# Kernel optimization log

Measured on AMD Instinct MI355X. Metric: run time of the kernel, lower is better.

The kernel has to match this reference:

```python
import jax, jax.numpy as jnp
import numpy as np

N_TAG = 128
START = 126  # tag2idx[START_TAG]
STOP = 127   # tag2idx[STOP_TAG]
NEG_INF = -10000.0


def setup_inputs() -> dict:
    key = jax.random.key(0)
    k1, k2, k3 = jax.random.split(key, 3)
    B, T = 512, 512
    feats = jax.random.normal(k1, (B, T, N_TAG), dtype=jnp.float32)
    transitions = jax.random.normal(k2, (N_TAG, N_TAG), dtype=jnp.float32)
    # __init__ constraints: no transition into START, none out of STOP
    transitions = transitions.at[START, :].set(NEG_INF)
    transitions = transitions.at[:, STOP].set(NEG_INF)
    tags = jax.random.randint(k3, (B, T), 0, 126, dtype=jnp.int32)
    return {"feats": feats, "transitions": transitions, "tags": tags}


def reference(feats, transitions, tags):
    # feats: [B, T, N], transitions[i, j] = score(j -> i), tags: [B, T]
    B, T, N = feats.shape

    # ---- forward algorithm (batched log-sum-exp DP) ----
    init = jnp.full((B, N), NEG_INF, dtype=feats.dtype).at[:, START].set(0.0)

    def step(fv, feat_t):  # fv: [B, N] (alpha over prev tag j), feat_t: [B, N]
        # tag_var[b, i, j] = fv[b, j] + transitions[i, j] + feat_t[b, i]
        tag_var = fv[:, None, :] + transitions[None, :, :] + feat_t[:, :, None]
        return jax.nn.logsumexp(tag_var, axis=2), None

    fv, _ = jax.lax.scan(step, init, jnp.swapaxes(feats, 0, 1))  # scan over T
    forward_score = jax.nn.logsumexp(fv + transitions[STOP][None, :], axis=1)  # [B]

    # ---- gold path score ----
    start_col = jnp.full((B, 1), START, dtype=tags.dtype)
    stop_col = jnp.full((B, 1), STOP, dtype=tags.dtype)
    pad_start = jnp.concatenate([start_col, tags], axis=1)  # from-tags, [B, T+1]
    pad_stop = jnp.concatenate([tags, stop_col], axis=1)    # to-tags,   [B, T+1]
    trans_score = transitions[pad_stop, pad_start].sum(axis=1)  # [B]
    emit_score = jnp.take_along_axis(feats, tags[:, :, None].astype(jnp.int32), axis=2)[..., 0].sum(axis=1)
    gold_score = trans_score + emit_score

    # negative log-likelihood per sequence
    return forward_score - gold_score
```

## Files before the change

### kernel.cpp

```cpp
#include <hip/hip_runtime.h>
#include <hip/hip_bf16.h>

#define N_TAG 128
#define T_LEN 512
#define START_TAG 126
#define STOP_TAG 127

typedef __attribute__((ext_vector_type(8))) __bf16 bf16x8;
typedef __attribute__((ext_vector_type(4))) float f32x4;

__global__ __launch_bounds__(320, 1)
void crf_split_kernel(const float* __restrict__ feats,
                      const float* __restrict__ trans,
                      const int* __restrict__ tags,
                      float* __restrict__ out) {
  const int tid = threadIdx.x;
  const int wid = tid >> 6;
  const int lane = tid & 63;
  const int bbase = blockIdx.x * 2;

  __shared__ float Uf[2][N_TAG];
  __shared__ float Wb[2][N_TAG];
  __shared__ float LZ[4];
  __shared__ float GOLD[2];

  if (wid == 4) {
    const int half = lane >> 5, tl = lane & 31;
    const int b = bbase + half;
    const int* tg = tags + (size_t)b * T_LEN;
    const float* fg = feats + (size_t)b * T_LEN * N_TAG;
    float gsum = 0.f;
    for (int t = tl; t < T_LEN; t += 32) {
      int tag = tg[t];
      int prev = (t == 0) ? START_TAG : tg[t - 1];
      gsum += trans[(size_t)tag * N_TAG + prev] + fg[(size_t)t * N_TAG + tag];
      if (t == T_LEN - 1) gsum += trans[STOP_TAG * N_TAG + tag];
    }
#pragma unroll
    for (int s = 16; s; s >>= 1) gsum += __shfl_xor(gsum, s);
    if (tl == 0) GOLD[half] = gsum;
    __syncthreads();
#pragma unroll
    for (int bL = 0; bL < 2; ++bL) {
      float sd = Uf[bL][lane] * Wb[bL][lane] +
                 Uf[bL][lane + 64] * Wb[bL][lane + 64];
#pragma unroll
      for (int s = 32; s; s >>= 1) sd += __shfl_xor(sd, s);
      if (lane == 0)
        out[bbase + bL] = __logf(sd) + LZ[2 * bL] + LZ[2 * bL + 1] - GOLD[bL];
    }
    return;
  }

  const int bL = wid >> 1, dir = wid & 1;
  const int batch = bbase + bL;
  const int n = lane & 15, g = lane >> 4;
  const float* fbase = feats + (size_t)batch * T_LEN * N_TAG;
  const int T0 = dir ? 510 : 0;
  const int TS = dir ? -1 : 1;
  const int ib = 32 * g;

  bf16x8 A[8][4];
#pragma unroll
  for (int mt = 0; mt < 8; ++mt) {
    const int tau = 32 * (mt >> 1) + 8 * (n >> 2) + 4 * (mt & 1) + (n & 3);
#pragma unroll
    for (int kk = 0; kk < 4; ++kk) {
      bf16x8 v;
      if (dir == 0) {
        const float* p = trans + (size_t)tau * N_TAG + 32 * kk + 8 * g;
        f32x4 x = *(const f32x4*)p;
        f32x4 y = *(const f32x4*)(p + 4);
        v[0] = (__bf16)__expf(x[0]); v[1] = (__bf16)__expf(x[1]);
        v[2] = (__bf16)__expf(x[2]); v[3] = (__bf16)__expf(x[3]);
        v[4] = (__bf16)__expf(y[0]); v[5] = (__bf16)__expf(y[1]);
        v[6] = (__bf16)__expf(y[2]); v[7] = (__bf16)__expf(y[3]);
      } else {
#pragma unroll
        for (int j = 0; j < 8; ++j)
          v[j] = (__bf16)__expf(trans[(size_t)(32 * kk + 8 * g + j) * N_TAG + tau]);
      }
      A[mt][kk] = v;
    }
  }

  bf16x8 Bv[4];
#pragma unroll
  for (int kk = 0; kk < 4; ++kk) {
    bf16x8 z;
#pragma unroll
    for (int j = 0; j < 8; ++j) z[j] = (__bf16)0.0f;
    Bv[kk] = z;
  }
  if (dir == 0) {
    if (g == 3) Bv[3][6] = (__bf16)1.0f;
  } else {
    const float* s127 = trans + (size_t)STOP_TAG * N_TAG;
    const float* f511 = fbase + (size_t)(T_LEN - 1) * N_TAG;
#pragma unroll
    for (int kk = 0; kk < 4; ++kk) {
      const int off = 32 * kk + 8 * g;
      f32x4 s0 = *(const f32x4*)(s127 + off);
      f32x4 s1 = *(const f32x4*)(s127 + off + 4);
      f32x4 e0 = *(const f32x4*)(f511 + off);
      f32x4 e1 = *(const f32x4*)(f511 + off + 4);
      bf16x8 v;
      v[0] = (__bf16)__expf(s0[0] + e0[0]); v[1] = (__bf16)__expf(s0[1] + e0[1]);
      v[2] = (__bf16)__expf(s0[2] + e0[2]); v[3] = (__bf16)__expf(s0[3] + e0[3]);
      v[4] = (__bf16)__expf(s1[0] + e1[0]); v[5] = (__bf16)__expf(s1[1] + e1[1]);
      v[6] = (__bf16)__expf(s1[2] + e1[2]); v[7] = (__bf16)__expf(s1[3] + e1[3]);
      Bv[kk] = v;
    }
  }

  float Lr[4][2];
#pragma unroll
  for (int s = 0; s < 4; ++s) {
    const float* rp = fbase + (size_t)(T0 + TS * s) * N_TAG;
    Lr[s][0] = rp[lane];
    Lr[s][1] = rp[lane + 64];
  }
  Lr[0][0] = __expf(Lr[0][0]);
  Lr[0][1] = __expf(Lr[0][1]);
  float logZ = 0.0f;

#define BPERM(DST, SLOT)                                                     \
  {                                                                          \
    _Pragma("unroll") for (int a = 0; a < 4; ++a) {                          \
      int sv_ = __float_as_int((a < 2) ? Lr[SLOT][0] : Lr[SLOT][1]);         \
      _Pragma("unroll") for (int bb = 0; bb < 2; ++bb) {                     \
        _Pragma("unroll") for (int r = 0; r < 4; ++r) {                      \
          int w_ = __builtin_amdgcn_ds_bpermute(                             \
              ib + 128 * (a & 1) + 16 * bb + 4 * r, sv_);                    \
          DST[2 * a + bb][r] = __int_as_float(w_);                           \
        }                                                                    \
      }                                                                      \
    }                                                                        \
  }

#define RENORM(ACC)                                                          \
  {                                                                          \
    float mx_ = ACC[0][0];                                                   \
    _Pragma("unroll") for (int mt = 0; mt < 8; ++mt)                         \
        mx_ = fmaxf(mx_, fmaxf(fmaxf(ACC[mt][0], ACC[mt][1]),                \
                               fmaxf(ACC[mt][2], ACC[mt][3])));              \
    mx_ = fmaxf(mx_, __shfl_xor(mx_, 16));                                   \
    mx_ = fmaxf(mx_, __shfl_xor(mx_, 32));                                   \
    int eb_ = __float_as_int(mx_) & 0x7f800000;                              \
    float inv_ = __int_as_float(0x7f000000 - eb_);           \
    logZ += (float)((eb_ >> 23) - 127) * 0.69314718056f;                     \
    _Pragma("unroll") for (int mt = 0; mt < 8; ++mt) {                       \
      ACC[mt][0] *= inv_; ACC[mt][1] *= inv_;                                \
      ACC[mt][2] *= inv_; ACC[mt][3] *= inv_;                                \
    }                                                                        \
  }

#define ITER(S, SX, KP4, DOREN)                                              \
  {                                                                          \
    f32x4 EF[8];                                                             \
    BPERM(EF, S);                                                            \
    f32x4 acc[8];                                                            \
    _Pragma("unroll") for (int mt = 0; mt < 8; ++mt)                         \
        acc[mt] = (f32x4){0.f, 0.f, 0.f, 0.f};                               \
    _Pragma("unroll") for (int kk = 0; kk < 4; ++kk) {                       \
      _Pragma("unroll") for (int mt = 0; mt < 8; ++mt)                       \
          acc[mt] = __builtin_amdgcn_mfma_f32_16x16x32_bf16(                 \
              A[mt][kk], Bv[kk], acc[mt], 0, 0, 0);                          \
    }                                                                        \
    _Pragma("unroll") for (int mt = 0; mt < 8; ++mt) {                       \
      acc[mt][0] *= EF[mt][0]; acc[mt][1] *= EF[mt][1];                      \
      acc[mt][2] *= EF[mt][2]; acc[mt][3] *= EF[mt][3];                      \
    }                                                                        \
    if (DOREN) RENORM(acc);                                                  \
    _Pragma("unroll") for (int kk = 0; kk < 4; ++kk) {                       \
      bf16x8 nb;                                                             \
      nb[0] = (__bf16)acc[2 * kk][0];     nb[1] = (__bf16)acc[2 * kk][1];    \
      nb[2] = (__bf16)acc[2 * kk][2];     nb[3] = (__bf16)acc[2 * kk][3];    \
      nb[4] = (__bf16)acc[2 * kk + 1][0]; nb[5] = (__bf16)acc[2 * kk + 1][1];\
      nb[6] = (__bf16)acc[2 * kk + 1][2]; nb[7] = (__bf16)acc[2 * kk + 1][3];\
      Bv[kk] = nb;                                                           \
    }                                                                        \
    Lr[SX][0] = __expf(Lr[SX][0]);  \
    Lr[SX][1] = __expf(Lr[SX][1]);                                           \
    {                                                                        \
      const float* rp_ = fbase + (size_t)(T0 + TS * (KP4)) * N_TAG;          \
      Lr[S][0] = rp_[lane];               \
      Lr[S][1] = rp_[lane + 64];                                             \
    }                                                                        \
  }

  for (int kb = 0; kb < 63; ++kb) {
    const int k0 = kb * 4;
    ITER(0, 1, k0 + 4, false);
    ITER(1, 2, k0 + 5, false);
    ITER(2, 3, k0 + 6, false);
    ITER(3, 0, k0 + 7, true);
  }
  ITER(0, 1, 256, false);
  ITER(1, 2, 257, false);
  ITER(2, 3, 258, false);

  f32x4 upF[8];
  {
    f32x4 EF[8];
    BPERM(EF, 3);
    f32x4 acc[8];
#pragma unroll
    for (int mt = 0; mt < 8; ++mt) acc[mt] = (f32x4){0.f, 0.f, 0.f, 0.f};
#pragma unroll
    for (int kk = 0; kk < 4; ++kk) {
#pragma unroll
      for (int mt = 0; mt < 8; ++mt)
        acc[mt] = __builtin_amdgcn_mfma_f32_16x16x32_bf16(A[mt][kk], Bv[kk],
                                                          acc[mt], 0, 0, 0);
    }
    if (dir == 0) {
#pragma unroll
      for (int mt = 0; mt < 8; ++mt) {
        acc[mt][0] *= EF[mt][0]; acc[mt][1] *= EF[mt][1];
        acc[mt][2] *= EF[mt][2]; acc[mt][3] *= EF[mt][3];
      }
    }
    RENORM(acc);
#pragma unroll
    for (int mt = 0; mt < 8; ++mt) upF[mt] = acc[mt];
  }

  float* dst = (dir == 0) ? Uf[bL] : Wb[bL];
  if (n == 0) {
#pragma unroll
    for (int mt = 0; mt < 8; ++mt) {
      const int base = 32 * (mt >> 1) + 8 * g + 4 * (mt & 1);
#pragma unroll
      for (int r = 0; r < 4; ++r) dst[base + r] = upF[mt][r];
    }
  }
  if (lane == 0) LZ[wid] = logZ;
  __syncthreads();
#undef ITER
#undef RENORM
#undef BPERM
}

extern "C" void kernel_launch(void* const* d_in, const int* in_sizes, int n_in,
                              void* d_out, int out_size, void* d_ws, size_t ws_size,
                              hipStream_t stream) {
  const float* feats = (const float*)d_in[0];
  const float* trans = (const float*)d_in[1];
  const int* tags = (const int*)d_in[2];
  float* out = (float*)d_out;
  int B = in_sizes[0] / (T_LEN * N_TAG);
  crf_split_kernel<<<B / 2, 320, 0, stream>>>(feats, trans, tags, out);
}
```

Before: 148.8 us.

## Stage emission rows into LDS via async global_load_lds double buffering

Result: slower. 280.4 us (+88.4%).

```diff
diff --git a/kernel.cpp b/kernel.cpp
--- a/kernel.cpp
+++ b/kernel.cpp
@@ -19,6 +19,7 @@
   const int lane = tid & 63;
   const int bbase = blockIdx.x * 2;
 
+  __shared__ __align__(16) float stage_lds[4][2][2048];
   __shared__ float Uf[2][N_TAG];
   __shared__ float Wb[2][N_TAG];
   __shared__ float LZ[4];
@@ -56,9 +57,6 @@
   const int batch = bbase + bL;
   const int n = lane & 15, g = lane >> 4;
   const float* fbase = feats + (size_t)batch * T_LEN * N_TAG;
-  const int T0 = dir ? 510 : 0;
-  const int TS = dir ? -1 : 1;
-  const int ib = 32 * g;
 
   bf16x8 A[8][4];
 #pragma unroll
@@ -113,113 +111,136 @@
     }
   }
 
-  float Lr[4][2];
-#pragma unroll
-  for (int s = 0; s < 4; ++s) {
-    const float* rp = fbase + (size_t)(T0 + TS * s) * N_TAG;
-    Lr[s][0] = rp[lane];
-    Lr[s][1] = rp[lane + 64];
-  }
-  Lr[0][0] = __expf(Lr[0][0]);
-  Lr[0][1] = __expf(Lr[0][1]);
+  const f32x4 FZ = {0.f, 0.f, 0.f, 0.f};
   float logZ = 0.0f;
-
-#define BPERM(DST, SLOT)                                                     \
-  {                                                                          \
-    _Pragma("unroll") for (int a = 0; a < 4; ++a) {                          \
-      int sv_ = __float_as_int((a < 2) ? Lr[SLOT][0] : Lr[SLOT][1]);         \
-      _Pragma("unroll") for (int bb = 0; bb < 2; ++bb) {                     \
-        _Pragma("unroll") for (int r = 0; r < 4; ++r) {                      \
-          int w_ = __builtin_amdgcn_ds_bpermute(                             \
-              ib + 128 * (a & 1) + 16 * bb + 4 * r, sv_);                    \
-          DST[2 * a + bb][r] = __int_as_float(w_);                           \
-        }                                                                    \
-      }                                                                      \
-    }                                                                        \
+  f32x4 upF[8];
+
+#define STAGE(M_)                                                             \
+  {                                                                           \
+    const int br_ = dir ? (495 - 16 * (M_)) : (16 * (M_));                    \
+    const float* gs_ = fbase + (size_t)br_ * N_TAG + lane * 4;                \
+    float* lb_ = &stage_lds[wid][(M_) & 1][0];                                \
+    _Pragma("unroll") for (int i_ = 0; i_ < 8; ++i_)                          \
+        __builtin_amdgcn_global_load_lds(                                     \
+            (const __attribute__((address_space(1))) unsigned int*)(gs_ +     \
+                                                                    i_ * 256),\
+            (__attribute__((address_space(3))) unsigned int*)(lb_ + i_ * 256),\
+            16, 0, 0);                                                        \
   }
 
 #define RENORM(ACC)                                                          \
   {                                                                          \
     float mx_ = ACC[0][0];                                                   \
-    _Pragma("unroll") for (int mt = 0; mt < 8; ++mt)                         \
-        mx_ = fmaxf(mx_, fmaxf(fmaxf(ACC[mt][0], ACC[mt][1]),                \
-                               fmaxf(ACC[mt][2], ACC[mt][3])));              \
+    _Pragma("unroll") for (int mt_ = 0; mt_ < 8; ++mt_)                      \
+        mx_ = fmaxf(mx_, fmaxf(fmaxf(ACC[mt_][0], ACC[mt_][1]),              \
+                               fmaxf(ACC[mt_][2], ACC[mt_][3])));            \
     mx_ = fmaxf(mx_, __shfl_xor(mx_, 16));                                   \
     mx_ = fmaxf(mx_, __shfl_xor(mx_, 32));                                   \
     int eb_ = __float_as_int(mx_) & 0x7f800000;                              \
     float inv_ = __int_as_float(0x7f000000 - eb_);           \
     logZ += (float)((eb_ >> 23) - 127) * 0.69314718056f;                     \
-    _Pragma("unroll") for (int mt = 0; mt < 8; ++mt) {                       \
-      ACC[mt][0] *= inv_; ACC[mt][1] *= inv_;                                \
-      ACC[mt][2] *= inv_; ACC[mt][3] *= inv_;                                \
+    _Pragma("unroll") for (int mt_ = 0; mt_ < 8; ++mt_) {                    \
+      ACC[mt_][0] *= inv_; ACC[mt_][1] *= inv_;                              \
+      ACC[mt_][2] *= inv_; ACC[mt_][3] *= inv_;                              \
     }                                                                        \
   }
 
-#define ITER(S, SX, KP4, DOREN)                                              \
+#define PACKB(ACC)                                                           \
   {                                                                          \
-    f32x4 EF[8];                                                             \
-    BPERM(EF, S);                                                            \
-    f32x4 acc[8];                                                            \
-    _Pragma("unroll") for (int mt = 0; mt < 8; ++mt)                         \
-        acc[mt] = (f32x4){0.f, 0.f, 0.f, 0.f};                               \
-    _Pragma("unroll") for (int kk = 0; kk < 4; ++kk) {                       \
-      _Pragma("unroll") for (int mt = 0; mt < 8; ++mt)                       \
-          acc[mt] = __builtin_amdgcn_mfma_f32_16x16x32_bf16(                 \
-              A[mt][kk], Bv[kk], acc[mt], 0, 0, 0);                          \
+    _Pragma("unroll") for (int kk_ = 0; kk_ < 4; ++kk_) {                    \
+      bf16x8 nb_;                                                            \
+      nb_[0] = (__bf16)ACC[2 * kk_][0];     nb_[1] = (__bf16)ACC[2 * kk_][1];\
+      nb_[2] = (__bf16)ACC[2 * kk_][2];     nb_[3] = (__bf16)ACC[2 * kk_][3];\
+      nb_[4] = (__bf16)ACC[2 * kk_ + 1][0]; nb_[5] = (__bf16)ACC[2 * kk_ + 1][1];\
+      nb_[6] = (__bf16)ACC[2 * kk_ + 1][2]; nb_[7] = (__bf16)ACC[2 * kk_ + 1][3];\
+      Bv[kk_] = nb_;                                                         \
     }                                                                        \
-    _Pragma("unroll") for (int mt = 0; mt < 8; ++mt) {                       \
-      acc[mt][0] *= EF[mt][0]; acc[mt][1] *= EF[mt][1];                      \
-      acc[mt][2] *= EF[mt][2]; acc[mt][3] *= EF[mt][3];                      \
+  }
+
+#define STEP(BUF, SOFF, DOREN)                                               \
+  {                                                                          \
+    const f32x4* row_ = (const f32x4*)&stage_lds[wid][BUF][(SOFF) * 128];    \
+    f32x4 Qv_[8];                                                            \
+    _Pragma("unroll") for (int a_ = 0; a_ < 4; ++a_)                         \
+        _Pragma("unroll") for (int bb_ = 0; bb_ < 2; ++bb_)                  \
+            Qv_[2 * a_ + bb_] = row_[8 * a_ + 2 * g + bb_];                  \
+    f32x4 acc_[8];                                                           \
+    _Pragma("unroll") for (int mt_ = 0; mt_ < 8; ++mt_)                      \
+        acc_[mt_] = __builtin_amdgcn_mfma_f32_16x16x32_bf16(A[mt_][0], Bv[0],\
+                                                            FZ, 0, 0, 0);    \
+    _Pragma("unroll") for (int kk_ = 1; kk_ < 4; ++kk_)                      \
+        _Pragma("unroll") for (int mt_ = 0; mt_ < 8; ++mt_)                  \
+            acc_[mt_] = __builtin_amdgcn_mfma_f32_16x16x32_bf16(             \
+                A[mt_][kk_], Bv[kk_], acc_[mt_], 0, 0, 0);                   \
+    _Pragma("unroll") for (int mt_ = 0; mt_ < 8; ++mt_) {                    \
+      acc_[mt_][0] *= __expf(Qv_[mt_][0]);                                   \
+      acc_[mt_][1] *= __expf(Qv_[mt_][1]);                                   \
+      acc_[mt_][2] *= __expf(Qv_[mt_][2]);                                   \
+      acc_[mt_][3] *= __expf(Qv_[mt_][3]);                                   \
     }                                                                        \
-    if (DOREN) RENORM(acc);                                                  \
-    _Pragma("unroll") for (int kk = 0; kk < 4; ++kk) {                       \
-      bf16x8 nb;                                                             \
-      nb[0] = (__bf16)acc[2 * kk][0];     nb[1] = (__bf16)acc[2 * kk][1];    \
-      nb[2] = (__bf16)acc[2 * kk][2];     nb[3] = (__bf16)acc[2 * kk][3];    \
-      nb[4] = (__bf16)acc[2 * kk + 1][0]; nb[5] = (__bf16)acc[2 * kk + 1][1];\
-      nb[6] = (__bf16)acc[2 * kk + 1][2]; nb[7] = (__bf16)acc[2 * kk + 1][3];\
-      Bv[kk] = nb;                                                           \
-    }                                                                        \
-    Lr[SX][0] = __expf(Lr[SX][0]);  \
-    Lr[SX][1] = __expf(Lr[SX][1]);                                           \
-    {                                                                        \
-      const float* rp_ = fbase + (size_t)(T0 + TS * (KP4)) * N_TAG;          \
-      Lr[S][0] = rp_[lane];               \
-      Lr[S][1] = rp_[lane + 64];                                             \
-    }                                                                        \
-  }
-
-  for (int kb = 0; kb < 63; ++kb) {
-    const int k0 = kb * 4;
-    ITER(0, 1, k0 + 4, false);
-    ITER(1, 2, k0 + 5, false);
-    ITER(2, 3, k0 + 6, false);
-    ITER(3, 0, k0 + 7, true);
-  }
-  ITER(0, 1, 256, false);
-  ITER(1, 2, 257, false);
-  ITER(2, 3, 258, false);
-
-  f32x4 upF[8];
+    if (DOREN) RENORM(acc_);                                                 \
+    PACKB(acc_);                                                             \
+  }
+
+  STAGE(0);
+  STAGE(1);
+
+  for (int m = 0; m < 15; ++m) {
+    asm volatile("s_waitcnt vmcnt(8)" ::: "memory");
+    const int bufc = m & 1;
+#pragma unroll
+    for (int q = 0; q < 4; ++q) {
+      {
+        const int o0 = 4 * q + 0, s0 = dir ? 15 - o0 : o0;
+        STEP(bufc, s0, false);
+      }
+      {
+        const int o1 = 4 * q + 1, s1 = dir ? 15 - o1 : o1;
+        STEP(bufc, s1, false);
+      }
+      {
+        const int o2 = 4 * q + 2, s2 = dir ? 15 - o2 : o2;
+        STEP(bufc, s2, false);
+      }
+      {
+        const int o3 = 4 * q + 3, s3 = dir ? 15 - o3 : o3;
+        STEP(bufc, s3, true);
+      }
+    }
+    asm volatile("s_waitcnt lgkmcnt(0)" ::: "memory");
+    if (m + 2 <= 15) STAGE(m + 2);
+  }
+
+  asm volatile("s_waitcnt vmcnt(0)" ::: "memory");
+#pragma unroll
+  for (int o = 0; o < 15; ++o) {
+    const int s = dir ? 15 - o : o;
+    STEP(1, s, (o & 3) == 3);
+  }
   {
-    f32x4 EF[8];
-    BPERM(EF, 3);
     f32x4 acc[8];
 #pragma unroll
-    for (int mt = 0; mt < 8; ++mt) acc[mt] = (f32x4){0.f, 0.f, 0.f, 0.f};
-#pragma unroll
-    for (int kk = 0; kk < 4; ++kk) {
+    for (int mt = 0; mt < 8; ++mt)
+      acc[mt] = __builtin_amdgcn_mfma_f32_16x16x32_bf16(A[mt][0], Bv[0], FZ,
+                                                        0, 0, 0);
+#pragma unroll
+    for (int kk = 1; kk < 4; ++kk)
 #pragma unroll
       for (int mt = 0; mt < 8; ++mt)
         acc[mt] = __builtin_amdgcn_mfma_f32_16x16x32_bf16(A[mt][kk], Bv[kk],
                                                           acc[mt], 0, 0, 0);
-    }
     if (dir == 0) {
-#pragma unroll
-      for (int mt = 0; mt < 8; ++mt) {
-        acc[mt][0] *= EF[mt][0]; acc[mt][1] *= EF[mt][1];
-        acc[mt][2] *= EF[mt][2]; acc[mt][3] *= EF[mt][3];
-      }
+      const f32x4* row = (const f32x4*)&stage_lds[wid][1][15 * 128];
+#pragma unroll
+      for (int a = 0; a < 4; ++a)
+#pragma unroll
+        for (int bb = 0; bb < 2; ++bb) {
+          f32x4 q = row[8 * a + 2 * g + bb];
+          acc[2 * a + bb][0] *= __expf(q[0]);
+          acc[2 * a + bb][1] *= __expf(q[1]);
+          acc[2 * a + bb][2] *= __expf(q[2]);
+          acc[2 * a + bb][3] *= __expf(q[3]);
+        }
     }
     RENORM(acc);
 #pragma unroll
@@ -237,9 +258,10 @@
   }
   if (lane == 0) LZ[wid] = logZ;
   __syncthreads();
-#undef ITER
+#undef STEP
+#undef PACKB
 #undef RENORM
-#undef BPERM
+#undef STAGE
 }
 
 extern "C" void kernel_launch(void* const* d_in, const int* in_sizes, int n_in,
```
